# Kernel tuning notes

Measured on AMD Instinct MI355X. Metric: run time of the kernel, lower is better.

Reference implementation:

```python
import jax, jax.numpy as jnp
import numpy as np

N, D, E, TOP_K = 4096, 1024, 8, 2
NEG_INF = -1e38


def setup_inputs() -> dict:
    key = jax.random.key(0)
    ks = jax.random.split(key, 6)
    s = 1.0 / np.sqrt(D)
    return {
        "x": jax.random.normal(ks[0], (N, D), jnp.float32),
        "noise": jax.random.normal(ks[1], (E,), jnp.float32),
        "Wg": jax.random.normal(ks[2], (D, E), jnp.float32) * s,
        "Wn": jax.random.normal(ks[3], (D, E), jnp.float32) * s,
        "We": jax.random.normal(ks[4], (E, D, D), jnp.float32) * s,
        "be": jax.random.normal(ks[5], (E, D), jnp.float32) * 0.01,
    }


def reference(x, noise, Wg, Wn, We, be):
    # Gating: H = Wg(x) + randn(E) * softplus(Wnoise(x))   (Eq. 4-5)
    g = x @ Wg                                      # [N, E]
    H = g + noise[None, :] * jax.nn.softplus(x @ Wn)  # [N, E]
    # Keep top_k entries of H, set the rest to -Inf (scatter of bottom E-k)
    vals, idx = jax.lax.top_k(H, TOP_K)             # [N, k]
    keep = jnp.full_like(H, NEG_INF)
    keep = keep.at[jnp.arange(H.shape[0])[:, None], idx].set(vals)
    G = jax.nn.softmax(keep, axis=1)                # [N, E]; masked entries -> 0
    # Expert outputs; masked experts have G==0 so dense weighted sum matches
    # the sparse per-example loop: out_n = sum_j G[n,j] * expert_j(x_n)
    Y = jnp.einsum('nd,edh->neh', x, We) + be[None, :, :]  # [N, E, D]
    out = jnp.einsum('ne,neh->nh', G, Y)            # [N, D]
    return out
```

## Files before the change

kernel.cpp:

```cpp
#include <hip/hip_runtime.h>
#include <hip/hip_bf16.h>
#include <stdint.h>

#define NR   4096
#define DIM  1024
#define NE   8
#define BM   128
#define BN   128
#define GBK  64

typedef __attribute__((ext_vector_type(8))) short  bf16x8;
typedef __attribute__((ext_vector_type(8))) ushort u16x8;
typedef __attribute__((ext_vector_type(4))) float  f32x4;

__device__ __forceinline__ ushort f2bf(float f) {
    union { __hip_bfloat16 h; ushort u; } cv;
    cv.h = __float2bfloat16(f);
    return cv.u;
}

__device__ __forceinline__ void gload16(const void* g, void* l) {
    __builtin_amdgcn_global_load_lds(
        (const __attribute__((address_space(1))) unsigned int*)g,
        (__attribute__((address_space(3))) unsigned int*)l, 16, 0, 0);
}

__global__ __launch_bounds__(256)
void k1_main(const float* __restrict__ We, ushort* __restrict__ WeT,
             const float* __restrict__ x, const float* __restrict__ noise,
             const float* __restrict__ Wg, const float* __restrict__ Wn,
             ushort* __restrict__ xbf,
             uint32_t* __restrict__ eid, float2* __restrict__ wpair) {
    __shared__ float smem[64 * 68];
    const int tid = threadIdx.x;
    if (blockIdx.x < 2048) {
        const int b  = blockIdx.x;
        const int e  = b >> 8, kt = (b >> 4) & 15, ct = b & 15;
        const float* src = We + ((size_t)e * DIM + (size_t)kt * 64) * DIM + ct * 64;
#pragma unroll
        for (int j = 0; j < 4; ++j) {
            int idx = tid + j * 256;
            int r = idx >> 4, c4 = idx & 15;
            *(float4*)&smem[r * 68 + c4 * 4] = *(const float4*)(src + (size_t)r * DIM + c4 * 4);
        }
        __syncthreads();
        ushort* dst = WeT + ((size_t)e * DIM + (size_t)ct * 64) * DIM + kt * 64;
#pragma unroll
        for (int j = 0; j < 2; ++j) {
            int u = tid + j * 256;
            int c = u >> 3, ch = u & 7;
            ushort tmp[8];
#pragma unroll
            for (int q = 0; q < 8; ++q) tmp[q] = f2bf(smem[(ch * 8 + q) * 68 + c]);
            *(u16x8*)(dst + (size_t)c * DIM + ch * 8) = *(u16x8*)tmp;
        }
    } else {
        const int w = tid >> 6, l = tid & 63;
        const int row = (blockIdx.x - 2048) * 4 + w;
        const float* xr = x + (size_t)row * DIM;
        ushort*     xbr = xbf + (size_t)row * DIM;

        float ag[8], an[8];
#pragma unroll
        for (int e = 0; e < 8; ++e) { ag[e] = 0.f; an[e] = 0.f; }

#pragma unroll
        for (int j = 0; j < 16; ++j) {
            const int k = j * 64 + l;
            float xv = xr[k];
            xbr[k] = f2bf(xv);
            const float4* g4 = (const float4*)(Wg + (size_t)k * NE);
            const float4* n4 = (const float4*)(Wn + (size_t)k * NE);
            float4 g0 = g4[0], g1 = g4[1], n0 = n4[0], n1 = n4[1];
            ag[0] += xv * g0.x; ag[1] += xv * g0.y; ag[2] += xv * g0.z; ag[3] += xv * g0.w;
            ag[4] += xv * g1.x; ag[5] += xv * g1.y; ag[6] += xv * g1.z; ag[7] += xv * g1.w;
            an[0] += xv * n0.x; an[1] += xv * n0.y; an[2] += xv * n0.z; an[3] += xv * n0.w;
            an[4] += xv * n1.x; an[5] += xv * n1.y; an[6] += xv * n1.z; an[7] += xv * n1.w;
        }
#pragma unroll
        for (int u = 0; u < 16; ++u)
            smem[(w * 64 + l) * 17 + u] = (u < 8) ? ag[u] : an[u - 8];
        asm volatile("s_waitcnt lgkmcnt(0)" ::: "memory");
        const int c = l >> 4, u = l & 15;
        float v = 0.f;
#pragma unroll
        for (int i = 0; i < 16; ++i) v += smem[(w * 64 + c * 16 + i) * 17 + u];
        v += __shfl_xor(v, 16, 64);
        v += __shfl_xor(v, 32, 64);

        const int e = l & 7;
        float agv = __shfl(v, e, 64);
        float anv = __shfl(v, e + 8, 64);
        float sp  = (anv > 0.f) ? (anv + log1pf(expf(-anv))) : log1pf(expf(anv));
        float H   = agv + noise[e] * sp;

        float Hh[8];
#pragma unroll
        for (int k = 0; k < 8; ++k) Hh[k] = __shfl(H, k, 64);
        if (l == 0) {
            int e0 = 0; float v0 = Hh[0];
#pragma unroll
            for (int k = 1; k < 8; ++k) if (Hh[k] > v0) { v0 = Hh[k]; e0 = k; }
            int e1 = -1; float v1 = 0.f;
#pragma unroll
            for (int k = 0; k < 8; ++k)
                if (k != e0 && (e1 < 0 || Hh[k] > v1)) { v1 = Hh[k]; e1 = k; }
            float rr = expf(v1 - v0);
            float w0 = 1.f / (1.f + rr), w1 = 1.f - w0;
            eid[row] = (uint32_t)e0 | ((uint32_t)e1 << 8);
            float2 wp; wp.x = w0; wp.y = w1;
            wpair[row] = wp;
        }
    }
}

__global__ __launch_bounds__(1024)
void bucket_build(const uint32_t* __restrict__ eid, const float2* __restrict__ wpair,
                  int* __restrict__ cnt, int* __restrict__ idxl, float* __restrict__ wl) {
    const int bucket = blockIdx.x;
    const int slot = bucket >> 3, ex = bucket & 7;
    __shared__ int base;
    __shared__ int wsum[16];
    if (threadIdx.x == 0) base = 0;
    const int wid = threadIdx.x >> 6, lane = threadIdx.x & 63;
    int* bidx = idxl + (size_t)bucket * NR;
    float* bwl = wl + (size_t)bucket * NR;

    for (int c0 = 0; c0 < NR; c0 += 1024) {
        const int row = c0 + threadIdx.x;
        const uint32_t em = eid[row];
        const int e = slot ? (int)((em >> 8) & 255u) : (int)(em & 255u);
        const bool m = (e == ex);
        const unsigned long long bal = __ballot(m);
        if (lane == 0) wsum[wid] = __popcll(bal);
        __syncthreads();
        int wbase = base;
        for (int i = 0; i < wid; ++i) wbase += wsum[i];
        const int pos = wbase + __popcll(bal & ((1ull << lane) - 1ull));
        if (m) {
            bidx[pos] = row;
            float2 wp = wpair[row];
            bwl[pos]  = slot ? wp.y : wp.x;
        }
        __syncthreads();
        if (threadIdx.x == 0) {
            int s = 0;
#pragma unroll
            for (int i = 0; i < 16; ++i) s += wsum[i];
            base += s;
        }
        __syncthreads();
    }
    if (threadIdx.x == 0) cnt[bucket] = base;
}

template<int PASS>
__global__ __launch_bounds__(256, 2)
void moe_gemm(const ushort* __restrict__ xbf, const ushort* __restrict__ WeT,
              const float* __restrict__ be, const int* __restrict__ cnt,
              const int* __restrict__ idxl, const float* __restrict__ wl,
              float* __restrict__ out) {
    __shared__ ushort Al[2][BM][GBK];
    __shared__ ushort Bl[2][BM][GBK];

    const int q8 = gridDim.x >> 3;
    const int W  = (blockIdx.x & 7) * q8 + (blockIdx.x >> 3);
    const int item = W >> 3, cT = W & 7;

    int bucket = -1, tile = 0, accp = 0;
#pragma unroll
    for (int b = 0; b < NE; ++b) {
        int t = (cnt[PASS * NE + b] + BM - 1) >> 7;
        if (bucket < 0 && item < accp + t) { bucket = PASS * NE + b; tile = item - accp; }
        accp += t;
    }
    if (bucket < 0) return;
    const int count  = cnt[bucket];
    const int nrowsv = min(BM, count - tile * BM);
    const int e  = bucket & 7;
    const int c0 = cT * BN;
    const int*   rows = idxl + (size_t)bucket * NR + tile * BM;
    const float* wrow = wl   + (size_t)bucket * NR + tile * BM;

    const int tid = threadIdx.x, wid = tid >> 6, lane = tid & 63;
    const int wr = (wid >> 1) * 64, wc = (wid & 1) * 64;
    const int l16 = lane & 15, lhi = lane >> 4;
    const int lr8 = lane >> 3, lc8 = lane & 7;
    const int chunkp = lc8 ^ lr8;

    const ushort* aptr[4];
    const ushort* bptr[4];
#pragma unroll
    for (int q = 0; q < 4; ++q) {
        int r  = wid * 32 + q * 8 + lr8;
        int gr = rows[min(r, nrowsv - 1)];
        aptr[q] = xbf + (size_t)gr * DIM + chunkp * 8;
        int c = c0 + wid * 32 + q * 8 + lr8;
        bptr[q] = WeT + ((size_t)(e * DIM + c)) * DIM + chunkp * 8;
    }

    f32x4 acc[4][4];
#pragma unroll
    for (int m = 0; m < 4; ++m)
#pragma unroll
        for (int n = 0; n < 4; ++n) { f32x4 z = {0.f, 0.f, 0.f, 0.f}; acc[m][n] = z; }

#pragma unroll
    for (int q = 0; q < 4; ++q) {
        gload16(aptr[q], &Al[0][wid * 32 + q * 8][0]);
        gload16(bptr[q], &Bl[0][wid * 32 + q * 8][0]);
    }

    for (int s = 0; s < DIM / GBK; ++s) {
        const int buf = s & 1;
        if (s + 1 < DIM / GBK) {
            const int nb = buf ^ 1, k0 = (s + 1) * GBK;
#pragma unroll
            for (int q = 0; q < 4; ++q) {
                gload16(aptr[q] + k0, &Al[nb][wid * 32 + q * 8][0]);
                gload16(bptr[q] + k0, &Bl[nb][wid * 32 + q * 8][0]);
            }
            asm volatile("s_waitcnt vmcnt(8)" ::: "memory");
        } else {
            asm volatile("s_waitcnt vmcnt(0)" ::: "memory");
        }
        __builtin_amdgcn_s_barrier();

        const ushort* Ab = &Al[buf][0][0];
        const ushort* Bb = &Bl[buf][0][0];
#pragma unroll
        for (int h = 0; h < 2; ++h) {
            bf16x8 af[4], bfr[4];
            const int chb = (h * 4 + lhi) ^ (l16 & 7);
#pragma unroll
            for (int m = 0; m < 4; ++m) {
                int rr = wr + m * 16 + l16;
                af[m] = *(const bf16x8*)(Ab + rr * GBK + chb * 8);
            }
#pragma unroll
            for (int n = 0; n < 4; ++n) {
                int rr = wc + n * 16 + l16;
                bfr[n] = *(const bf16x8*)(Bb + rr * GBK + chb * 8);
            }
#pragma unroll
            for (int m = 0; m < 4; ++m)
#pragma unroll
                for (int n = 0; n < 4; ++n)
                    acc[m][n] = __builtin_amdgcn_mfma_f32_16x16x32_bf16(af[m], bfr[n], acc[m][n], 0, 0, 0);
        }
        asm volatile("s_waitcnt lgkmcnt(0)" ::: "memory");
        __builtin_amdgcn_s_barrier();
    }

    float bev[4];
#pragma unroll
    for (int n = 0; n < 4; ++n) bev[n] = be[(size_t)e * DIM + c0 + wc + n * 16 + l16];
#pragma unroll
    for (int m = 0; m < 4; ++m) {
#pragma unroll
        for (int r = 0; r < 4; ++r) {
            int rl = wr + m * 16 + lhi * 4 + r;
            if (rl < nrowsv) {
                int   gr = rows[rl];
                float w  = wrow[rl];
                float* op = out + (size_t)gr * DIM + c0 + wc;
#pragma unroll
                for (int n = 0; n < 4; ++n) {
                    float v   = w * (acc[m][n][r] + bev[n]);
                    int   col = n * 16 + l16;
                    if (PASS == 0) op[col] = v;
                    else           op[col] += v;
                }
            }
        }
    }
}

extern "C" void kernel_launch(void* const* d_in, const int* in_sizes, int n_in,
                              void* d_out, int out_size, void* d_ws, size_t ws_size,
                              hipStream_t stream) {
    const float* x     = (const float*)d_in[0];
    const float* noise = (const float*)d_in[1];
    const float* Wg    = (const float*)d_in[2];
    const float* Wn    = (const float*)d_in[3];
    const float* We    = (const float*)d_in[4];
    const float* be    = (const float*)d_in[5];
    float* out = (float*)d_out;

    char* w = (char*)d_ws;
    size_t off = 256;
    int*      cnt   = (int*)w;
    int*      idxl  = (int*)(w + off);      off += (size_t)2 * NE * NR * 4;
    float*    wl    = (float*)(w + off);    off += (size_t)2 * NE * NR * 4;
    uint32_t* eid   = (uint32_t*)(w + off); off += (size_t)NR * 4;
    float2*   wpair = (float2*)(w + off);   off += (size_t)NR * 8;
    off = (off + 255) & ~(size_t)255;
    ushort* xbf = (ushort*)(w + off); off += (size_t)NR * DIM * 2;
    ushort* WeT = (ushort*)(w + off); off += (size_t)NE * DIM * DIM * 2;

    k1_main<<<3072, 256, 0, stream>>>(We, WeT, x, noise, Wg, Wn, xbf, eid, wpair);
    bucket_build<<<16, 1024, 0, stream>>>(eid, wpair, cnt, idxl, wl);
    moe_gemm<0><<<40 * 8, 256, 0, stream>>>(xbf, WeT, be, cnt, idxl, wl, out);
    moe_gemm<1><<<40 * 8, 256, 0, stream>>>(xbf, WeT, be, cnt, idxl, wl, out);
}
```

Baseline: 88.30 us.

## Merge both top-k expert GEMM passes into one launch with scratch buffer plus add

The two per-slot GEMM launches become a single launch covering all 16 buckets. The second slot's results go to a workspace buffer and are summed into the output by a separate elementwise kernel, so the slot-0 write and slot-1 read-modify-write no longer have to be serialized. Tile mapping now uses a fixed 32-tiles-per-bucket grid with early exit for empty tiles, replacing the prefix-sum search over bucket counts. This launches many idle blocks and adds an extra 16MB read and 16MB read-modify-write pass over the output. The gating kernel also switches to float4 loads of x, and the fallback path keeps two launches when workspace is too small.

```diff
diff --git a/kernel.cpp b/kernel.cpp
--- a/kernel.cpp
+++ b/kernel.cpp
@@ -58,24 +58,37 @@
         const int w = tid >> 6, l = tid & 63;
         const int row = (blockIdx.x - 2048) * 4 + w;
         const float* xr = x + (size_t)row * DIM;
-        ushort*     xbr = xbf + (size_t)row * DIM;
+
+        float4 xv[4];
+#pragma unroll
+        for (int q = 0; q < 4; ++q) xv[q] = *(const float4*)(xr + q * 256 + l * 4);
+#pragma unroll
+        for (int q = 0; q < 4; ++q) {
+            ushort4 xb;
+            xb.x = f2bf(xv[q].x); xb.y = f2bf(xv[q].y);
+            xb.z = f2bf(xv[q].z); xb.w = f2bf(xv[q].w);
+            *(ushort4*)(xbf + (size_t)row * DIM + q * 256 + l * 4) = xb;
+        }
 
         float ag[8], an[8];
 #pragma unroll
         for (int e = 0; e < 8; ++e) { ag[e] = 0.f; an[e] = 0.f; }
-
-#pragma unroll
-        for (int j = 0; j < 16; ++j) {
-            const int k = j * 64 + l;
-            float xv = xr[k];
-            xbr[k] = f2bf(xv);
-            const float4* g4 = (const float4*)(Wg + (size_t)k * NE);
-            const float4* n4 = (const float4*)(Wn + (size_t)k * NE);
-            float4 g0 = g4[0], g1 = g4[1], n0 = n4[0], n1 = n4[1];
-            ag[0] += xv * g0.x; ag[1] += xv * g0.y; ag[2] += xv * g0.z; ag[3] += xv * g0.w;
-            ag[4] += xv * g1.x; ag[5] += xv * g1.y; ag[6] += xv * g1.z; ag[7] += xv * g1.w;
-            an[0] += xv * n0.x; an[1] += xv * n0.y; an[2] += xv * n0.z; an[3] += xv * n0.w;
-            an[4] += xv * n1.x; an[5] += xv * n1.y; an[6] += xv * n1.z; an[7] += xv * n1.w;
+#pragma unroll
+        for (int q = 0; q < 4; ++q) {
+            const int k0 = q * 256 + l * 4;
+            const float4* gp = (const float4*)(Wg + (size_t)k0 * NE);
+            const float4* np = (const float4*)(Wn + (size_t)k0 * NE);
+            const float4 xq = xv[q];
+#pragma unroll
+            for (int ik = 0; ik < 4; ++ik) {
+                const float xs = (ik == 0) ? xq.x : (ik == 1) ? xq.y : (ik == 2) ? xq.z : xq.w;
+                float4 g0 = gp[2 * ik], g1 = gp[2 * ik + 1];
+                float4 n0 = np[2 * ik], n1 = np[2 * ik + 1];
+                ag[0] += xs * g0.x; ag[1] += xs * g0.y; ag[2] += xs * g0.z; ag[3] += xs * g0.w;
+                ag[4] += xs * g1.x; ag[5] += xs * g1.y; ag[6] += xs * g1.z; ag[7] += xs * g1.w;
+                an[0] += xs * n0.x; an[1] += xs * n0.y; an[2] += xs * n0.z; an[3] += xs * n0.w;
+                an[4] += xs * n1.x; an[5] += xs * n1.y; an[6] += xs * n1.z; an[7] += xs * n1.w;
+            }
         }
 #pragma unroll
         for (int u = 0; u < 16; ++u)
@@ -154,33 +167,27 @@
     if (threadIdx.x == 0) cnt[bucket] = base;
 }
 
-template<int PASS>
 __global__ __launch_bounds__(256, 2)
 void moe_gemm(const ushort* __restrict__ xbf, const ushort* __restrict__ WeT,
               const float* __restrict__ be, const int* __restrict__ cnt,
               const int* __restrict__ idxl, const float* __restrict__ wl,
-              float* __restrict__ out) {
+              float* __restrict__ out, float* __restrict__ y1,
+              int bucket0, int use_y1) {
     __shared__ ushort Al[2][BM][GBK];
     __shared__ ushort Bl[2][BM][GBK];
 
     const int q8 = gridDim.x >> 3;
     const int W  = (blockIdx.x & 7) * q8 + (blockIdx.x >> 3);
-    const int item = W >> 3, cT = W & 7;
-
-    int bucket = -1, tile = 0, accp = 0;
-#pragma unroll
-    for (int b = 0; b < NE; ++b) {
-        int t = (cnt[PASS * NE + b] + BM - 1) >> 7;
-        if (bucket < 0 && item < accp + t) { bucket = PASS * NE + b; tile = item - accp; }
-        accp += t;
-    }
-    if (bucket < 0) return;
-    const int count  = cnt[bucket];
-    const int nrowsv = min(BM, count - tile * BM);
+    const int bucket = bucket0 + (W >> 8);
+    const int t  = (W >> 3) & 31;
+    const int cT = W & 7;
+    const int count = cnt[bucket];
+    if (t * BM >= count) return;
+    const int nrowsv = min(BM, count - t * BM);
     const int e  = bucket & 7;
     const int c0 = cT * BN;
-    const int*   rows = idxl + (size_t)bucket * NR + tile * BM;
-    const float* wrow = wl   + (size_t)bucket * NR + tile * BM;
+    const int*   rows = idxl + (size_t)bucket * NR + t * BM;
+    const float* wrow = wl   + (size_t)bucket * NR + t * BM;
 
     const int tid = threadIdx.x, wid = tid >> 6, lane = tid & 63;
     const int wr = (wid >> 1) * 64, wc = (wid & 1) * 64;
@@ -252,6 +259,8 @@
         __builtin_amdgcn_s_barrier();
     }
 
+    float* dst = (bucket >= NE && use_y1) ? y1 : out;
+    const bool accum = (bucket >= NE) && !use_y1;
     float bev[4];
 #pragma unroll
     for (int n = 0; n < 4; ++n) bev[n] = be[(size_t)e * DIM + c0 + wc + n * 16 + l16];
@@ -263,16 +272,26 @@
             if (rl < nrowsv) {
                 int   gr = rows[rl];
                 float w  = wrow[rl];
-                float* op = out + (size_t)gr * DIM + c0 + wc;
+                float* op = dst + (size_t)gr * DIM + c0 + wc;
 #pragma unroll
                 for (int n = 0; n < 4; ++n) {
                     float v   = w * (acc[m][n][r] + bev[n]);
                     int   col = n * 16 + l16;
-                    if (PASS == 0) op[col] = v;
-                    else           op[col] += v;
+                    if (accum) op[col] += v; else op[col] = v;
                 }
             }
         }
+    }
+}
+
+__global__ __launch_bounds__(256)
+void add_out(float* __restrict__ out, const float* __restrict__ y1) {
+    const int n4 = NR * DIM / 4;
+    for (int i = blockIdx.x * blockDim.x + threadIdx.x; i < n4; i += gridDim.x * blockDim.x) {
+        float4 a = ((float4*)out)[i];
+        float4 b = ((const float4*)y1)[i];
+        a.x += b.x; a.y += b.y; a.z += b.z; a.w += b.w;
+        ((float4*)out)[i] = a;
     }
 }
 
@@ -297,9 +316,18 @@
     off = (off + 255) & ~(size_t)255;
     ushort* xbf = (ushort*)(w + off); off += (size_t)NR * DIM * 2;
     ushort* WeT = (ushort*)(w + off); off += (size_t)NE * DIM * DIM * 2;
+    float*  y1  = (float*)(w + off);
+    size_t need_y1 = off + (size_t)NR * DIM * 4;
+    const int use_y1 = (ws_size >= need_y1) ? 1 : 0;
 
     k1_main<<<3072, 256, 0, stream>>>(We, WeT, x, noise, Wg, Wn, xbf, eid, wpair);
     bucket_build<<<16, 1024, 0, stream>>>(eid, wpair, cnt, idxl, wl);
-    moe_gemm<0><<<40 * 8, 256, 0, stream>>>(xbf, WeT, be, cnt, idxl, wl, out);
-    moe_gemm<1><<<40 * 8, 256, 0, stream>>>(xbf, WeT, be, cnt, idxl, wl, out);
-}
+
+    if (use_y1) {
+        moe_gemm<<<16 * 32 * 8, 256, 0, stream>>>(xbf, WeT, be, cnt, idxl, wl, out, y1, 0, 1);
+        add_out<<<2048, 256, 0, stream>>>(out, y1);
+    } else {
+        moe_gemm<<<8 * 32 * 8, 256, 0, stream>>>(xbf, WeT, be, cnt, idxl, wl, out, nullptr, 0, 0);
+        moe_gemm<<<8 * 32 * 8, 256, 0, stream>>>(xbf, WeT, be, cnt, idxl, wl, out, nullptr, 8, 0);
+    }
+}
```

New measurement: 102.6 us. +16.2%, slower.
